# Performance work log

Hardware: AMD Instinct MI355X
Metric: run time of the kernel (lower is better)

The kernel has to match this reference:

```python
import jax, jax.numpy as jnp
import numpy as np

I, T, L, E, H, W = 256, 256, 32, 128, 7, 7

def setup_inputs() -> dict:
    key = jax.random.key(0)
    k1, k2, k3 = jax.random.split(key, 3)
    image_features = jax.random.normal(k1, (I, E, H, W), dtype=jnp.float32)
    text_features = jax.random.normal(k2, (T, L, E), dtype=jnp.float32)
    text_length = jax.random.randint(k3, (T,), 1, L + 1, dtype=jnp.int32)
    logit_neg_log_temperature = jnp.asarray(-np.log(0.07), dtype=jnp.float32)
    return {
        "image_features": image_features,
        "text_features": text_features,
        "text_length": text_length,
        "logit_neg_log_temperature": logit_neg_log_temperature,
    }

def reference(image_features, text_features, text_length, logit_neg_log_temperature):
    # image_features: [I, E, H, W]; text_features: [T, L, E]
    i, e, h, w = image_features.shape
    img = image_features.reshape(i, e, h * w)            # [I, E, HW]
    # cross-modal similarity per (image, text, token, patch): [I, T, L, HW]
    sim = jnp.einsum('iep,tle->itlp', img, text_features)
    # max over patches, then sum over tokens, normalized by caption length
    match_max = jnp.max(sim, axis=3)                     # [I, T, L]
    match = jnp.sum(match_max, axis=2) / text_length.astype(match_max.dtype)  # [I, T]
    logit_scale = jnp.exp(logit_neg_log_temperature)
    logits_per_image = match * logit_scale
    logits_per_text = match.T * logit_scale
    return (logits_per_image, logits_per_text)
```

## Files before the change

kernel.cpp:

```cpp
#include <hip/hip_runtime.h>
#include <hip/hip_bf16.h>

typedef __attribute__((ext_vector_type(8))) short bf16x8;
typedef __attribute__((ext_vector_type(4))) float f32x4;

#define I_N 256
#define T_N 256
#define L_N 32
#define E_N 128
#define P_N 49
#define TG  4

__global__ __launch_bounds__(256) void pack_all(const float* __restrict__ txt,
                                                const float* __restrict__ img,
                                                unsigned short* __restrict__ bpre,
                                                unsigned short* __restrict__ apre) {
    const int bid = blockIdx.x;
    if (bid < 512) {
        int gid  = bid * 256 + threadIdx.x;
        int lane = gid & 63;
        int kk   = (gid >> 6) & 3;
        int tt   = gid >> 8;
        int row  = tt * 16 + (lane & 15);
        int e0   = kk * 32 + (lane >> 4) * 8;
        const float* src = txt + row * E_N + e0;
        union { unsigned short u[8]; bf16x8 v; } o;
        #pragma unroll
        for (int j = 0; j < 8; ++j) {
            __hip_bfloat16 h = __float2bfloat16(src[j]);
            o.u[j] = *reinterpret_cast<unsigned short*>(&h);
        }
        ((bf16x8*)bpre)[gid] = o.v;
    } else {
        int gid   = (bid - 512) * 256 + threadIdx.x;
        int lane  = gid & 63;
        int kk    = (gid >> 6) & 3;
        int pt    = (gid >> 8) & 3;
        int i     = gid >> 10;
        int patch = pt * 16 + (lane & 15);
        int e0    = kk * 32 + (lane >> 4) * 8;
        const float* src = img + i * (E_N * P_N) + e0 * P_N + patch;
        union { unsigned short u[8]; bf16x8 v; } o;
        #pragma unroll
        for (int j = 0; j < 8; ++j) {
            float x = (patch < P_N) ? src[j * P_N] : 0.0f;
            __hip_bfloat16 h = __float2bfloat16(x);
            o.u[j] = *reinterpret_cast<unsigned short*>(&h);
        }
        ((bf16x8*)apre)[gid] = o.v;
    }
}

__global__ __launch_bounds__(512) void clip_mfma(
    const unsigned short* __restrict__ apre,
    const unsigned short* __restrict__ bpre,
    const int*   __restrict__ tlen,
    const float* __restrict__ nlt,
    float*       __restrict__ out) {

    __shared__ short sB[2][TG * 8 * 64 * 8];

    const int wid  = threadIdx.x >> 6;
    const int lane = threadIdx.x & 63;
    const int i    = blockIdx.y * 8 + wid;
    const int t0   = blockIdx.x * 16;
    const float scale = expf(nlt[0]);
    const bool  lo16  = (lane < 16);

    bf16x8 af[4][4];
    const bf16x8* ap = (const bf16x8*)apre + (size_t)i * 16 * 64;
    #pragma unroll
    for (int pt = 0; pt < 4; ++pt)
        #pragma unroll
        for (int kk = 0; kk < 4; ++kk)
            af[pt][kk] = ap[(pt * 4 + kk) * 64 + lane];

    auto stage = [&](int buf, int g) {
        #pragma unroll
        for (int q = 0; q < 4; ++q) {
            int fl = wid * 4 + q;
            int t  = t0 + g * TG + (fl >> 3);
            int f  = fl & 7;
            const unsigned short* src = bpre + ((size_t)(t * 8 + f)) * 512 + lane * 8;
            short* dst = &sB[buf][fl * 512];
            __builtin_amdgcn_global_load_lds(
                (const __attribute__((address_space(1))) unsigned int*)(const void*)src,
                (__attribute__((address_space(3))) unsigned int*)(void*)dst, 16, 0, 0);
        }
    };

    stage(0, 0);
    __syncthreads();

    #pragma unroll 1
    for (int g = 0; g < 4; ++g) {
        const int cur = g & 1;
        if (g < 3) stage(cur ^ 1, g + 1);

        const bf16x8* bfp = (const bf16x8*)&sB[cur][0];
        #pragma unroll
        for (int tx = 0; tx < TG; ++tx) {
            bf16x8 bf[2][4];
            #pragma unroll
            for (int ctt = 0; ctt < 2; ++ctt)
                #pragma unroll
                for (int kk = 0; kk < 4; ++kk)
                    bf[ctt][kk] = bfp[(tx * 8 + ctt * 4 + kk) * 64 + lane];

            f32x4 acc[4][2];
            #pragma unroll
            for (int pt = 0; pt < 4; ++pt)
                #pragma unroll
                for (int ctt = 0; ctt < 2; ++ctt)
                    acc[pt][ctt] = (f32x4){0.f, 0.f, 0.f, 0.f};

            #pragma unroll
            for (int kk = 0; kk < 4; ++kk)
                #pragma unroll
                for (int pt = 0; pt < 4; ++pt)
                    #pragma unroll
                    for (int ctt = 0; ctt < 2; ++ctt)
                        acc[pt][ctt] = __builtin_amdgcn_mfma_f32_16x16x32_bf16(
                            af[pt][kk], bf[ctt][kk], acc[pt][ctt], 0, 0, 0);

            float colmax[2];
            #pragma unroll
            for (int ctt = 0; ctt < 2; ++ctt) {
                float m[4];
                #pragma unroll
                for (int r = 0; r < 4; ++r)
                    m[r] = fmaxf(fmaxf(acc[0][ctt][r], acc[1][ctt][r]), acc[2][ctt][r]);
                m[0] = fmaxf(m[0], lo16 ? acc[3][ctt][0] : -INFINITY);
                float mm = fmaxf(fmaxf(m[0], m[1]), fmaxf(m[2], m[3]));
                mm = fmaxf(mm, __shfl_xor(mm, 16));
                mm = fmaxf(mm, __shfl_xor(mm, 32));
                colmax[ctt] = mm;
            }
            float s = colmax[0] + colmax[1];
            #pragma unroll
            for (int off = 1; off <= 8; off <<= 1)
                s += __shfl_xor(s, off);

            const int t = t0 + g * TG + tx;
            if (lane == 0) {
                float match = (s / (float)tlen[t]) * scale;
                out[i * T_N + t]             = match;
                out[I_N * T_N + t * I_N + i] = match;
            }
        }
        __syncthreads();
    }
}

extern "C" void kernel_launch(void* const* d_in, const int* in_sizes, int n_in,
                              void* d_out, int out_size, void* d_ws, size_t ws_size,
                              hipStream_t stream) {
    const float* img  = (const float*)d_in[0];
    const float* txt  = (const float*)d_in[1];
    const int*   tlen = (const int*)d_in[2];
    const float* nlt  = (const float*)d_in[3];
    float*       out  = (float*)d_out;

    unsigned short* bpre = (unsigned short*)d_ws;
    unsigned short* apre = (unsigned short*)((char*)d_ws + (2u << 20));

    pack_all<<<1536, 256, 0, stream>>>(txt, img, bpre, apre);

    dim3 grid(16, 32);
    clip_mfma<<<grid, 512, 0, stream>>>(apre, bpre, tlen, nlt, out);
}
```

Baseline: 47.32 us.

## Software-pipeline MFMA and max-reduction across text tiles with double-buffered accumulators

Fully unrolls the 16 text tiles per block and keeps two accumulator/fragment sets. The shuffle-based max/sum reduction of tile t-1 is issued after the MFMAs of tile t. This should let the reduction overlap MFMA latency instead of stalling on it. Barrier placement is reworked so staging happens every four tiles, at the cost of higher register pressure from the doubled accumulators and fragments.

```diff
diff --git a/kernel.cpp b/kernel.cpp
--- a/kernel.cpp
+++ b/kernel.cpp
@@ -58,7 +58,7 @@
     const float* __restrict__ nlt,
     float*       __restrict__ out) {
 
-    __shared__ short sB[2][TG * 8 * 64 * 8];
+    __shared__ short sB[2][TG * 8 * 512];
 
     const int wid  = threadIdx.x >> 6;
     const int lane = threadIdx.x & 63;
@@ -89,67 +89,73 @@
         }
     };
 
+    auto reduceT = [&](f32x4 (&a)[4][2], int t) {
+        float colmax[2];
+        #pragma unroll
+        for (int ctt = 0; ctt < 2; ++ctt) {
+            float m[4];
+            #pragma unroll
+            for (int r = 0; r < 4; ++r)
+                m[r] = fmaxf(fmaxf(a[0][ctt][r], a[1][ctt][r]), a[2][ctt][r]);
+            m[0] = fmaxf(m[0], lo16 ? a[3][ctt][0] : -INFINITY);
+            float mm = fmaxf(fmaxf(m[0], m[1]), fmaxf(m[2], m[3]));
+            mm = fmaxf(mm, __shfl_xor(mm, 16));
+            mm = fmaxf(mm, __shfl_xor(mm, 32));
+            colmax[ctt] = mm;
+        }
+        float s = colmax[0] + colmax[1];
+        #pragma unroll
+        for (int off = 1; off <= 8; off <<= 1)
+            s += __shfl_xor(s, off);
+        if (lane == 0) {
+            float match = (s / (float)tlen[t]) * scale;
+            out[i * T_N + t]             = match;
+            out[I_N * T_N + t * I_N + i] = match;
+        }
+    };
+
+    bf16x8 bf[2][2][4];
+    f32x4  acc[2][4][2];
+
     stage(0, 0);
     __syncthreads();
 
-    #pragma unroll 1
-    for (int g = 0; g < 4; ++g) {
-        const int cur = g & 1;
-        if (g < 3) stage(cur ^ 1, g + 1);
+    #pragma unroll
+    for (int tx = 0; tx < 16; ++tx) {
+        const int p   = tx & 1;
+        const int gg  = tx >> 2;
+        const int txg = tx & 3;
 
-        const bf16x8* bfp = (const bf16x8*)&sB[cur][0];
+        if ((tx & 3) == 0) {
+            if (tx > 0) __syncthreads();
+            if (gg + 1 < 4) stage((gg + 1) & 1, gg + 1);
+        }
+
+        const bf16x8* bfp = (const bf16x8*)&sB[gg & 1][0];
         #pragma unroll
-        for (int tx = 0; tx < TG; ++tx) {
-            bf16x8 bf[2][4];
+        for (int ctt = 0; ctt < 2; ++ctt)
+            #pragma unroll
+            for (int kk = 0; kk < 4; ++kk)
+                bf[p][ctt][kk] = bfp[(txg * 8 + ctt * 4 + kk) * 64 + lane];
+
+        #pragma unroll
+        for (int pt = 0; pt < 4; ++pt)
             #pragma unroll
             for (int ctt = 0; ctt < 2; ++ctt)
-                #pragma unroll
-                for (int kk = 0; kk < 4; ++kk)
-                    bf[ctt][kk] = bfp[(tx * 8 + ctt * 4 + kk) * 64 + lane];
+                acc[p][pt][ctt] = (f32x4){0.f, 0.f, 0.f, 0.f};
 
-            f32x4 acc[4][2];
+        #pragma unroll
+        for (int kk = 0; kk < 4; ++kk)
             #pragma unroll
             for (int pt = 0; pt < 4; ++pt)
                 #pragma unroll
                 for (int ctt = 0; ctt < 2; ++ctt)
-                    acc[pt][ctt] = (f32x4){0.f, 0.f, 0.f, 0.f};
+                    acc[p][pt][ctt] = __builtin_amdgcn_mfma_f32_16x16x32_bf16(
+                        af[pt][kk], bf[p][ctt][kk], acc[p][pt][ctt], 0, 0, 0);
 
-            #pragma unroll
-            for (int kk = 0; kk < 4; ++kk)
-                #pragma unroll
-                for (int pt = 0; pt < 4; ++pt)
-                    #pragma unroll
-                    for (int ctt = 0; ctt < 2; ++ctt)
-                        acc[pt][ctt] = __builtin_amdgcn_mfma_f32_16x16x32_bf16(
-                            af[pt][kk], bf[ctt][kk], acc[pt][ctt], 0, 0, 0);
-
-            float colmax[2];
-            #pragma unroll
-            for (int ctt = 0; ctt < 2; ++ctt) {
-                float m[4];
-                #pragma unroll
-                for (int r = 0; r < 4; ++r)
-                    m[r] = fmaxf(fmaxf(acc[0][ctt][r], acc[1][ctt][r]), acc[2][ctt][r]);
-                m[0] = fmaxf(m[0], lo16 ? acc[3][ctt][0] : -INFINITY);
-                float mm = fmaxf(fmaxf(m[0], m[1]), fmaxf(m[2], m[3]));
-                mm = fmaxf(mm, __shfl_xor(mm, 16));
-                mm = fmaxf(mm, __shfl_xor(mm, 32));
-                colmax[ctt] = mm;
-            }
-            float s = colmax[0] + colmax[1];
-            #pragma unroll
-            for (int off = 1; off <= 8; off <<= 1)
-                s += __shfl_xor(s, off);
-
-            const int t = t0 + g * TG + tx;
-            if (lane == 0) {
-                float match = (s / (float)tlen[t]) * scale;
-                out[i * T_N + t]             = match;
-                out[I_N * T_N + t * I_N + i] = match;
-            }
-        }
-        __syncthreads();
+        if (tx > 0) reduceT(acc[1 - p], t0 + tx - 1);
     }
+    reduceT(acc[1], t0 + 15);
 }
 
 extern "C" void kernel_launch(void* const* d_in, const int* in_sizes, int n_in,
```

New measurement: 45.54 us. 3.8% less time.
